# Kernel optimization log

Measured on AMD Instinct MI355X. Metric: run time of the kernel, lower is better.

Reference implementation:

```python
import jax, jax.numpy as jnp
import numpy as np
from jax import lax

VOCAB, H, B, T = 2514, 300, 128, 512

def setup_inputs() -> dict:
    key = jax.random.key(0)
    ks = jax.random.split(key, 12)
    s = 1.0 / np.sqrt(H)
    inp = {
        'x': jax.random.randint(ks[0], (B, T), 0, VOCAB),
        'emb': jax.random.normal(ks[1], (VOCAB, H), jnp.float32),
        'Wih0': jax.random.uniform(ks[2], (4 * H, H), jnp.float32, -s, s),
        'Whh0': jax.random.uniform(ks[3], (4 * H, H), jnp.float32, -s, s),
        'bih0': jax.random.uniform(ks[4], (4 * H,), jnp.float32, -s, s),
        'bhh0': jax.random.uniform(ks[5], (4 * H,), jnp.float32, -s, s),
        'Wih1': jax.random.uniform(ks[6], (4 * H, H), jnp.float32, -s, s),
        'Whh1': jax.random.uniform(ks[7], (4 * H, H), jnp.float32, -s, s),
        'bih1': jax.random.uniform(ks[8], (4 * H,), jnp.float32, -s, s),
        'bhh1': jax.random.uniform(ks[9], (4 * H,), jnp.float32, -s, s),
        'Wout': jax.random.uniform(ks[10], (VOCAB, H), jnp.float32, -s, s),
        'bout': jax.random.uniform(ks[11], (VOCAB,), jnp.float32, -s, s),
    }
    return inp


def lstm_layer(x, Wih, Whh, bih, bhh):
    # x: [B, T, H] -> [B, T, H]. PyTorch gate order: i, f, g, o.
    b, t, _ = x.shape
    h = Whh.shape[1]
    xg = jnp.einsum('bti,gi->btg', x, Wih) + (bih + bhh)  # [B, T, 4H]
    h0 = jnp.zeros((b, h), x.dtype)
    c0 = jnp.zeros((b, h), x.dtype)

    def step(carry, g_t):
        hp, cp = carry
        gates = g_t + hp @ Whh.T
        i, f, g, o = jnp.split(gates, 4, axis=-1)
        c = jax.nn.sigmoid(f) * cp + jax.nn.sigmoid(i) * jnp.tanh(g)
        hh = jax.nn.sigmoid(o) * jnp.tanh(c)
        return (hh, c), hh

    _, ys = lax.scan(step, (h0, c0), jnp.swapaxes(xg, 0, 1))  # [T, B, H]
    return jnp.swapaxes(ys, 0, 1)


def reference(x, emb, Wih0, Whh0, bih0, bhh0, Wih1, Whh1, bih1, bhh1, Wout, bout):
    e = emb[x]                                   # [B, T, H]
    h1 = lstm_layer(e, Wih0, Whh0, bih0, bhh0)   # layer 1
    h2 = lstm_layer(h1, Wih1, Whh1, bih1, bhh1)  # layer 2
    logits = jnp.einsum('bth,vh->btv', h2, Wout) + bout
    return logits.reshape(-1, logits.shape[-1])  # [B*T, VOCAB]
```

## Files before the change

kernel.cpp:

```cpp
#include <hip/hip_runtime.h>
#include <cstdint>
#include <cstddef>

namespace {

constexpr int H    = 300;
constexpr int B    = 128;
constexpr int T    = 512;
constexpr int NVOC = 2514;
constexpr int KP   = 304;

typedef __attribute__((ext_vector_type(8))) short  short8;
typedef __attribute__((ext_vector_type(4))) float  f32x4;

__device__ __forceinline__ float sigm(float x)     { return 1.f / (1.f + __expf(-x)); }
__device__ __forceinline__ float tanhfast(float x) { return 1.f - 2.f / (__expf(2.f*x) + 1.f); }

__device__ __forceinline__ unsigned short bf16_rn(float f) {
    unsigned u = __float_as_uint(f);
    u += 0x7FFFu + ((u >> 16) & 1u);
    return (unsigned short)(u >> 16);
}
__device__ __forceinline__ float bf16_f(unsigned short s) {
    return __uint_as_float(((unsigned)s) << 16);
}
__device__ __forceinline__ unsigned pack_hl(float v) {
    const unsigned short hi = bf16_rn(v);
    const unsigned short lo = bf16_rn(v - bf16_f(hi));
    return (unsigned)hi | ((unsigned)lo << 16);
}

constexpr int TSEG = 15 * 128 * 20;

constexpr unsigned SENTP = 0x7FB07FB0u;

__global__ __launch_bounds__(256)
void sentinel_fill(uint4* __restrict__ p, size_t n4)
{
    const uint4 s = make_uint4(SENTP, SENTP, SENTP, SENTP);
    size_t i = (size_t)blockIdx.x * blockDim.x + threadIdx.x;
    const size_t stride = (size_t)gridDim.x * blockDim.x;
    for (; i < n4; i += stride) p[i] = s;
}

__global__ __launch_bounds__(256)
void preconv(const float* __restrict__ src, unsigned* __restrict__ dst, int rows)
{
    const size_t n = (size_t)rows * KP;
    for (size_t i = (size_t)blockIdx.x * 256 + threadIdx.x; i < n;
         i += (size_t)gridDim.x * 256) {
        const int c = (int)(i % KP), r = (int)(i / KP);
        dst[i] = (c < H) ? pack_hl(src[(size_t)r * H + c]) : 0u;
    }
}

__global__ __launch_bounds__(256)
void gemm_pk(const unsigned* __restrict__ Apk, const unsigned* __restrict__ Wpk,
             const float* __restrict__ b1, float* __restrict__ out, int N)
{
    __shared__ __align__(16) unsigned short Ah[128][40], Al[128][40];
    __shared__ __align__(16) unsigned short Wh[128][40];

    const int tid = threadIdx.x;
    const int tt = blockIdx.y;
    const int n0 = blockIdx.x * 128;
    const int rl = tid >> 1, cb = (tid & 1) * 16;

    const unsigned* aptr = Apk + (size_t)tt * TSEG + rl * 20;
    const int nrow = n0 + rl;
    const unsigned* wptr = Wpk + (size_t)nrow * KP;
    const bool nok = (nrow < N);

    const int wv = tid >> 6, lane = tid & 63;
    const int mw = (wv >> 1) * 64, nw = (wv & 1) * 64;
    const int kg = lane >> 4, mm = lane & 15;

    f32x4 acc[4][4];
#pragma unroll
    for (int i = 0; i < 4; ++i)
#pragma unroll
        for (int j = 0; j < 4; ++j) acc[i][j] = (f32x4){0.f, 0.f, 0.f, 0.f};

    for (int kt = 0; kt < 10; ++kt) {
        uint4 pa[4], pw[4];
#pragma unroll
        for (int j = 0; j < 4; ++j) {
            const int col = kt * 32 + cb + j * 4;
            pa[j] = (col < 300)
                  ? *(const uint4*)(aptr + (col / 20) * 2560 + col % 20)
                  : make_uint4(0, 0, 0, 0);
            pw[j] = (nok && col < KP) ? *(const uint4*)(wptr + col)
                                      : make_uint4(0, 0, 0, 0);
        }
        __syncthreads();
#pragma unroll
        for (int j = 0; j < 4; ++j) {
            const int cc = cb + j * 4;
            *(uint2*)&Ah[rl][cc] = make_uint2((pa[j].x & 0xFFFFu) | (pa[j].y << 16),
                                              (pa[j].z & 0xFFFFu) | (pa[j].w << 16));
            *(uint2*)&Al[rl][cc] = make_uint2((pa[j].x >> 16) | (pa[j].y & 0xFFFF0000u),
                                              (pa[j].z >> 16) | (pa[j].w & 0xFFFF0000u));
            *(uint2*)&Wh[rl][cc] = make_uint2((pw[j].x & 0xFFFFu) | (pw[j].y << 16),
                                              (pw[j].z & 0xFFFFu) | (pw[j].w << 16));
        }
        __syncthreads();

        short8 fah[4], fal[4], fbh[4];
#pragma unroll
        for (int f = 0; f < 4; ++f) {
            fah[f] = *(const short8*)&Ah[mw + f*16 + mm][kg*8];
            fal[f] = *(const short8*)&Al[mw + f*16 + mm][kg*8];
            fbh[f] = *(const short8*)&Wh[nw + f*16 + mm][kg*8];
        }
#pragma unroll
        for (int mf = 0; mf < 4; ++mf)
#pragma unroll
            for (int nf = 0; nf < 4; ++nf) {
                acc[mf][nf] = __builtin_amdgcn_mfma_f32_16x16x32_bf16(fah[mf], fbh[nf], acc[mf][nf], 0, 0, 0);
                acc[mf][nf] = __builtin_amdgcn_mfma_f32_16x16x32_bf16(fal[mf], fbh[nf], acc[mf][nf], 0, 0, 0);
            }
    }

    float bias[4];
#pragma unroll
    for (int nf = 0; nf < 4; ++nf) {
        const int n = n0 + nw + nf*16 + mm;
        bias[nf] = (n < N) ? b1[n] : 0.f;
    }
    const int qr = lane >> 4;
#pragma unroll
    for (int mf = 0; mf < 4; ++mf) {
        const int b0 = mw + mf*16 + qr*4;
        float* orow = out + ((size_t)b0 * T + tt) * N;
#pragma unroll
        for (int nf = 0; nf < 4; ++nf) {
            const int n = n0 + nw + nf*16 + mm;
            if (n < N) {
#pragma unroll
                for (int r = 0; r < 4; ++r)
                    orow[(size_t)r * T * N + n] = acc[mf][nf][r] + bias[nf];
            }
        }
    }
}

constexpr int HGC = 15;
constexpr int BGC = 16;
constexpr int NWG = HGC * BGC;
constexpr int A2OFF  = 20480;
constexpr int EOFF   = 40960;
constexpr int APARF  = 61440;
constexpr int GDOFF  = 2 * APARF;
constexpr int TOKOFF = GDOFF + 10*8*16*4;
constexpr int FLDS   = TOKOFF + 8*512*4;

struct StageCtx {
    size_t   src64[5];
    int      aoffHi[5];
    unsigned pend0;
};

__device__ __forceinline__ void stage_init(StageCtx& S, int lane, int bg,
                                           int base_hg, int nchunks, int region)
{
    const int words = nchunks * 80;
    S.pend0 = 0;
#pragma unroll
    for (int j = 0; j < 5; ++j) {
        const int s = lane + 64 * j;
        const bool ok = (s < words);
        const int chunk = ok ? s / 80 : 0, rem = ok ? s % 80 : 0;
        const int hg = base_hg + chunk;
        S.src64[j] = (size_t)(hg * 128 + bg * 8) * 10 + rem;
        const int u2 = rem * 2, b_loc = u2 / 20, u = u2 % 20;
        const int k = hg * 20 + u;
        S.aoffHi[j] = region + ((k >> 5) * 8 + ((k >> 3) & 3)) * 256
                    + b_loc * 16 + (k & 7) * 2;
        if (ok) S.pend0 |= 1u << j;
    }
}

__device__ __forceinline__ void stage_poll(const StageCtx& S,
                                           const unsigned* __restrict__ slice,
                                           unsigned char* Ap)
{
    const unsigned long long* s64 = (const unsigned long long*)slice;
    unsigned long long val[5];
    unsigned pend = S.pend0;
    while (__any(pend != 0)) {
        unsigned long long w[5];
#pragma unroll
        for (int j = 0; j < 5; ++j)
            if (pend & (1u << j))
                w[j] = __hip_atomic_load(s64 + S.src64[j], __ATOMIC_RELAXED,
                                         __HIP_MEMORY_SCOPE_AGENT);
#pragma unroll
        for (int j = 0; j < 5; ++j)
            if (pend & (1u << j)) {
                const unsigned long long x = w[j];
                if ((unsigned)x != SENTP && (unsigned)(x >> 32) != SENTP) {
                    val[j] = x; pend &= ~(1u << j);
                }
            }
    }
#pragma unroll
    for (int j = 0; j < 5; ++j)
        if (S.pend0 & (1u << j)) {
            const unsigned p0 = (unsigned)val[j], p1 = (unsigned)(val[j] >> 32);
            *(unsigned*)(Ap + S.aoffHi[j])        = (p0 & 0xFFFFu) | (p1 << 16);
            *(unsigned*)(Ap + S.aoffHi[j] + 1024) = (p0 >> 16) | (p1 & 0xFFFF0000u);
        }
}

struct ECtx { int b[3]; int koff[3]; int aoff[3]; bool ok[3]; };

__device__ __forceinline__ void estage_init(ECtx& E, int tid)
{
#pragma unroll
    for (int j = 0; j < 3; ++j) {
        const int es = tid + 512 * j;
        E.ok[j] = (es < 1216);
        const int bb = E.ok[j] ? es / 152 : 0;
        const int kp = E.ok[j] ? es % 152 : 0;
        const int k  = kp * 2;
        E.b[j]    = bb;
        E.koff[j] = k;
        E.aoff[j] = EOFF + ((k >> 5) * 8 + ((k >> 3) & 3)) * 256
                  + bb * 16 + (k & 7) * 2;
    }
}

__device__ __forceinline__ void estage(const ECtx& E, const int* __restrict__ tokL,
                                       const unsigned* __restrict__ embcv, int it,
                                       unsigned char* Ap)
{
#pragma unroll
    for (int j = 0; j < 3; ++j)
        if (E.ok[j]) {
            const int tok = tokL[E.b[j] * 512 + it];
            const unsigned long long w = *(const unsigned long long*)
                (embcv + (size_t)tok * KP + E.koff[j]);
            const unsigned p0 = (unsigned)w, p1 = (unsigned)(w >> 32);
            *(unsigned*)(Ap + E.aoff[j])        = (p0 & 0xFFFFu) | (p1 << 16);
            *(unsigned*)(Ap + E.aoff[j] + 1024) = (p0 >> 16) | (p1 & 0xFFFF0000u);
        }
}

__device__ void fused_L0(int lane, int nt, int hg, int bg,
                         const unsigned* __restrict__ embcv,
                         const float* __restrict__ Wih0,
                         const float* __restrict__ Whh0,
                         const float* __restrict__ bih0,
                         const float* __restrict__ bhh0,
                         unsigned* __restrict__ h1p,
                         const unsigned* __restrict__ ssrc, int sreg, int sbase,
                         int snch, int sdel,
                         const ECtx& E, const int* __restrict__ tokL,
                         unsigned char* __restrict__ Abuf, float (*gd)[8][16])
{
    const int kg = lane >> 4, mm = lane & 15;

    short8 bhh[10], bih[10], bil[10];
#pragma unroll
    for (int kt = 0; kt < 10; ++kt) {
        const int c = nt * 16 + mm;
        const int grow = (c & 3) * H + hg * 20 + (c >> 2);
        short8 h_, ih_, il_;
#pragma unroll
        for (int e = 0; e < 8; ++e) {
            const int k = kt * 32 + kg * 8 + e;
            const float vh = (k < H) ? Whh0[(size_t)grow * H + k] : 0.f;
            const float vi = (k < H) ? Wih0[(size_t)grow * H + k] : 0.f;
            h_[e] = (short)bf16_rn(vh);
            const unsigned short i16 = bf16_rn(vi);
            ih_[e] = (short)i16;
            il_[e] = (short)bf16_rn(vi - bf16_f(i16));
        }
        bhh[kt] = h_; bih[kt] = ih_; bil[kt] = il_;
    }

    StageCtx S; stage_init(S, lane, bg, sbase, snch, sreg);

    const bool upd = lane < 32;
    const int b_u = lane >> 2, u4 = lane & 3;
    const int u_loc = nt * 4 + u4;
    float bias[4];
#pragma unroll
    for (int g = 0; g < 4; ++g)
        bias[g] = bih0[g * H + hg * 20 + u_loc] + bhh0[g * H + hg * 20 + u_loc];
    float cst = 0.f;
    unsigned* hst = h1p + ((size_t)hg * 128 + bg * 8 + b_u) * 20 + u_loc;

    for (int it = 0; it <= T; ++it) {
        unsigned char* Ap = Abuf + (it & 1) * APARF;
        if (it < T) estage(E, tokL, embcv, it, Ap);
        if (it >= sdel) stage_poll(S, ssrc + (size_t)(it - sdel) * TSEG, Ap);
        __syncthreads();

        if (it < T) {
            f32x4 acc = (f32x4){0.f, 0.f, 0.f, 0.f};
#pragma unroll
            for (int kt = 0; kt < 10; ++kt) {
                const int boff = (kt * 8 + kg) * 256 + mm * 16;
                const short8 eh = *(const short8*)(Ap + EOFF + boff);
                const short8 el = *(const short8*)(Ap + EOFF + boff + 1024);
                const short8 hh = *(const short8*)(Ap + boff);
                const short8 hl = *(const short8*)(Ap + boff + 1024);
                acc = __builtin_amdgcn_mfma_f32_16x16x32_bf16(eh, bih[kt], acc, 0, 0, 0);
                acc = __builtin_amdgcn_mfma_f32_16x16x32_bf16(el, bih[kt], acc, 0, 0, 0);
                acc = __builtin_amdgcn_mfma_f32_16x16x32_bf16(eh, bil[kt], acc, 0, 0, 0);
                acc = __builtin_amdgcn_mfma_f32_16x16x32_bf16(hh, bhh[kt], acc, 0, 0, 0);
                acc = __builtin_amdgcn_mfma_f32_16x16x32_bf16(hl, bhh[kt], acc, 0, 0, 0);
            }
            if (lane < 32) {
                const int br = (lane >> 4) * 4;
#pragma unroll
                for (int r = 0; r < 4; ++r) gd[nt][br + r][mm] = acc[r];
            }
            if (upd) {
                const float* g4 = &gd[nt][b_u][u4 * 4];
                const float gi = bias[0] + g4[0], gf = bias[1] + g4[1];
                const float gz = bias[2] + g4[2], go = bias[3] + g4[3];
                const float iG = sigm(gi), fG = sigm(gf);
                const float zG = tanhfast(gz), oG = sigm(go);
                cst = fmaf(fG, cst, iG * zG);
                const float hv = oG * tanhfast(cst);
                __hip_atomic_store(hst + (size_t)it * TSEG, pack_hl(hv),
                                   __ATOMIC_RELAXED, __HIP_MEMORY_SCOPE_AGENT);
            }
        }
    }
}

template<int NTL>
__device__ void fused_L1(int lane, int t0, int hg, int bg,
                         const unsigned* __restrict__ embcv,
                         const float* __restrict__ Wih1,
                         const float* __restrict__ Whh1,
                         const float* __restrict__ bih1,
                         const float* __restrict__ bhh1,
                         unsigned* __restrict__ h2p,
                         const unsigned* __restrict__ ssrc, int sreg, int sbase,
                         int snch, int sdel,
                         const ECtx& E, const int* __restrict__ tokL,
                         unsigned char* __restrict__ Abuf, float (*gd)[8][16])
{
    const int kg = lane >> 4, mm = lane & 15;

    short8 bi[NTL][10], bh[NTL][10];
#pragma unroll
    for (int t = 0; t < NTL; ++t)
#pragma unroll
        for (int kt = 0; kt < 10; ++kt) {
            const int c = (t0 + t) * 16 + mm;
            const int grow = (c & 3) * H + hg * 20 + (c >> 2);
            short8 i_, h_;
#pragma unroll
            for (int e = 0; e < 8; ++e) {
                const int k = kt * 32 + kg * 8 + e;
                i_[e] = (short)bf16_rn((k < H) ? Wih1[(size_t)grow * H + k] : 0.f);
                h_[e] = (short)bf16_rn((k < H) ? Whh1[(size_t)grow * H + k] : 0.f);
            }
            bi[t][kt] = i_; bh[t][kt] = h_;
        }

    StageCtx S; stage_init(S, lane, bg, sbase, snch, sreg);

    const bool upd = lane < NTL * 32;
    const int tile = lane >> 5, lidx = lane & 31;
    const int b_u = lidx >> 2, u4 = lidx & 3;
    const int ntg = t0 + ((NTL > 1) ? tile : 0);
    const int u_loc = ntg * 4 + u4;
    float bias[4];
#pragma unroll
    for (int g = 0; g < 4; ++g)
        bias[g] = bih1[g * H + hg * 20 + u_loc] + bhh1[g * H + hg * 20 + u_loc];
    float cst = 0.f;
    unsigned* hst = h2p + ((size_t)hg * 128 + bg * 8 + b_u) * 20 + u_loc;

    for (int it = 0; it <= T; ++it) {
        unsigned char* Ap = Abuf + (it & 1) * APARF;
        if (it < T) estage(E, tokL, embcv, it, Ap);
        if (it >= sdel) stage_poll(S, ssrc + (size_t)(it - sdel) * TSEG, Ap);
        __syncthreads();

        if (it >= 1) {
            f32x4 acc[NTL];
#pragma unroll
            for (int t = 0; t < NTL; ++t) acc[t] = (f32x4){0.f, 0.f, 0.f, 0.f};
#pragma unroll
            for (int kt = 0; kt < 10; ++kt) {
                const int boff = (kt * 8 + kg) * 256 + mm * 16;
                const short8 x1h = *(const short8*)(Ap + boff);
                const short8 x1l = *(const short8*)(Ap + boff + 1024);
                const short8 x2h = *(const short8*)(Ap + A2OFF + boff);
                const short8 x2l = *(const short8*)(Ap + A2OFF + boff + 1024);
#pragma unroll
                for (int t = 0; t < NTL; ++t) {
                    acc[t] = __builtin_amdgcn_mfma_f32_16x16x32_bf16(x1h, bi[t][kt], acc[t], 0, 0, 0);
                    acc[t] = __builtin_amdgcn_mfma_f32_16x16x32_bf16(x1l, bi[t][kt], acc[t], 0, 0, 0);
                    acc[t] = __builtin_amdgcn_mfma_f32_16x16x32_bf16(x2h, bh[t][kt], acc[t], 0, 0, 0);
                    acc[t] = __builtin_amdgcn_mfma_f32_16x16x32_bf16(x2l, bh[t][kt], acc[t], 0, 0, 0);
                }
            }
            if (lane < 32) {
                const int br = (lane >> 4) * 4;
#pragma unroll
                for (int t = 0; t < NTL; ++t)
#pragma unroll
                    for (int r = 0; r < 4; ++r) gd[5 + t0 + t][br + r][mm] = acc[t][r];
            }
            if (upd) {
                const float* g4 = &gd[5 + ntg][b_u][u4 * 4];
                const float gi = bias[0] + g4[0], gf = bias[1] + g4[1];
                const float gz = bias[2] + g4[2], go = bias[3] + g4[3];
                const float iG = sigm(gi), fG = sigm(gf);
                const float zG = tanhfast(gz), oG = sigm(go);
                cst = fmaf(fG, cst, iG * zG);
                const float hv = oG * tanhfast(cst);
                __hip_atomic_store(hst + (size_t)(it - 1) * TSEG, pack_hl(hv),
                                   __ATOMIC_RELAXED, __HIP_MEMORY_SCOPE_AGENT);
            }
        }
    }
}

__global__ __launch_bounds__(512, 2)
void lstm_fused(const int* __restrict__ x,
                const unsigned* __restrict__ embcv,
                const float* __restrict__ Wih0, const float* __restrict__ Whh0,
                const float* __restrict__ bih0, const float* __restrict__ bhh0,
                const float* __restrict__ Wih1, const float* __restrict__ Whh1,
                const float* __restrict__ bih1, const float* __restrict__ bhh1,
                unsigned* __restrict__ h1p, unsigned* __restrict__ h2p)
{
    extern __shared__ unsigned char smem[];
    unsigned char* Abuf = smem;
    float (*gd)[8][16] = (float(*)[8][16])(smem + GDOFF);
    int* tokL = (int*)(smem + TOKOFF);

    const int tid = threadIdx.x, wv = tid >> 6, lane = tid & 63;
    const int hg = blockIdx.x % HGC, bg = blockIdx.x / HGC;

    for (int i = tid; i < FLDS / 16; i += 512)
        ((uint4*)smem)[i] = make_uint4(0, 0, 0, 0);
    __syncthreads();
    for (int idx = tid; idx < 8 * 512; idx += 512) {
        const int b = idx >> 9, tt = idx & 511;
        tokL[idx] = x[(size_t)(bg * 8 + b) * T + tt];
    }
    __syncthreads();

    ECtx E; estage_init(E, tid);

    const int      sreg  = (wv < 4) ? 0 : A2OFF;
    const unsigned* ssrc = (wv < 4) ? h1p : h2p;
    const int      sbase = (wv & 3) * 4;
    const int      snch  = ((wv & 3) == 3) ? 3 : 4;
    const int      sdel  = (wv < 4) ? 1 : 2;

    if (wv < 5)
        fused_L0(lane, wv, hg, bg, embcv, Wih0, Whh0, bih0, bhh0, h1p,
                 ssrc, sreg, sbase, snch, sdel, E, tokL, Abuf, gd);
    else if (wv == 5)
        fused_L1<2>(lane, 0, hg, bg, embcv, Wih1, Whh1, bih1, bhh1, h2p,
                    ssrc, sreg, sbase, snch, sdel, E, tokL, Abuf, gd);
    else if (wv == 6)
        fused_L1<2>(lane, 2, hg, bg, embcv, Wih1, Whh1, bih1, bhh1, h2p,
                    ssrc, sreg, sbase, snch, sdel, E, tokL, Abuf, gd);
    else
        fused_L1<1>(lane, 4, hg, bg, embcv, Wih1, Whh1, bih1, bhh1, h2p,
                    ssrc, sreg, sbase, snch, sdel, E, tokL, Abuf, gd);
}

}

extern "C" void kernel_launch(void* const* d_in, const int* in_sizes, int n_in,
                              void* d_out, int out_size, void* d_ws, size_t ws_size,
                              hipStream_t stream)
{
    const int*   x    = (const int*)  d_in[0];
    const float* emb  = (const float*)d_in[1];
    const float* Wih0 = (const float*)d_in[2];
    const float* Whh0 = (const float*)d_in[3];
    const float* bih0 = (const float*)d_in[4];
    const float* bhh0 = (const float*)d_in[5];
    const float* Wih1 = (const float*)d_in[6];
    const float* Whh1 = (const float*)d_in[7];
    const float* bih1 = (const float*)d_in[8];
    const float* bhh1 = (const float*)d_in[9];
    const float* Wout = (const float*)d_in[10];
    const float* bout = (const float*)d_in[11];

    float* out = (float*)d_out;

    unsigned* h1p   = (unsigned*)d_ws;
    unsigned* h2p   = h1p + (size_t)T * TSEG;
    unsigned* embcv = h2p + (size_t)T * TSEG;
    unsigned* wcvo  = embcv + (size_t)NVOC * KP;

    const size_t nh4 = 2 * (size_t)T * TSEG / 4;
    sentinel_fill<<<dim3(2048), dim3(256), 0, stream>>>((uint4*)h1p, nh4);
    preconv<<<dim3(256), dim3(256), 0, stream>>>(emb,  embcv, NVOC);
    preconv<<<dim3(256), dim3(256), 0, stream>>>(Wout, wcvo,  NVOC);

    hipFuncSetAttribute(reinterpret_cast<const void*>(lstm_fused),
                        hipFuncAttributeMaxDynamicSharedMemorySize, FLDS);

    lstm_fused<<<dim3(NWG), dim3(512), FLDS, stream>>>(
        x, embcv, Wih0, Whh0, bih0, bhh0, Wih1, Whh1, bih1, bhh1, h1p, h2p);

    gemm_pk<<<dim3(20, 512), dim3(256), 0, stream>>>(h2p, wcvo, bout, out, NVOC);
}
```

Baseline: 3.061 ms.

## Fuse output projection GEMM into persistent LSTM kernel as per-step tail

Removes the separate output-projection GEMM launch. Each workgroup of the persistent LSTM kernel now computes the logits for its batch group and a slice of the vocabulary right after each timestep, reading the layer-2 hidden state already staged in shared memory. The Wout operand is stored as hi-only bf16 padded to 320 columns for direct MFMA fragment loads. This aims to overlap the projection with the serial recurrence and skip reloading h2 from global memory. The cost is extra per-step work and global output writes inside the latency-critical recurrent loop, plus two extra loop iterations.

```diff
diff --git a/kernel.cpp b/kernel.cpp
--- a/kernel.cpp
+++ b/kernel.cpp
@@ -9,6 +9,8 @@
 constexpr int T    = 512;
 constexpr int NVOC = 2514;
 constexpr int KP   = 304;
+constexpr int NTT  = 158;
+constexpr int NVP  = NTT * 16;
 
 typedef __attribute__((ext_vector_type(8))) short  short8;
 typedef __attribute__((ext_vector_type(4))) float  f32x4;
@@ -55,92 +57,14 @@
 }
 
 __global__ __launch_bounds__(256)
-void gemm_pk(const unsigned* __restrict__ Apk, const unsigned* __restrict__ Wpk,
-             const float* __restrict__ b1, float* __restrict__ out, int N)
-{
-    __shared__ __align__(16) unsigned short Ah[128][40], Al[128][40];
-    __shared__ __align__(16) unsigned short Wh[128][40];
-
-    const int tid = threadIdx.x;
-    const int tt = blockIdx.y;
-    const int n0 = blockIdx.x * 128;
-    const int rl = tid >> 1, cb = (tid & 1) * 16;
-
-    const unsigned* aptr = Apk + (size_t)tt * TSEG + rl * 20;
-    const int nrow = n0 + rl;
-    const unsigned* wptr = Wpk + (size_t)nrow * KP;
-    const bool nok = (nrow < N);
-
-    const int wv = tid >> 6, lane = tid & 63;
-    const int mw = (wv >> 1) * 64, nw = (wv & 1) * 64;
-    const int kg = lane >> 4, mm = lane & 15;
-
-    f32x4 acc[4][4];
-#pragma unroll
-    for (int i = 0; i < 4; ++i)
-#pragma unroll
-        for (int j = 0; j < 4; ++j) acc[i][j] = (f32x4){0.f, 0.f, 0.f, 0.f};
-
-    for (int kt = 0; kt < 10; ++kt) {
-        uint4 pa[4], pw[4];
-#pragma unroll
-        for (int j = 0; j < 4; ++j) {
-            const int col = kt * 32 + cb + j * 4;
-            pa[j] = (col < 300)
-                  ? *(const uint4*)(aptr + (col / 20) * 2560 + col % 20)
-                  : make_uint4(0, 0, 0, 0);
-            pw[j] = (nok && col < KP) ? *(const uint4*)(wptr + col)
-                                      : make_uint4(0, 0, 0, 0);
-        }
-        __syncthreads();
-#pragma unroll
-        for (int j = 0; j < 4; ++j) {
-            const int cc = cb + j * 4;
-            *(uint2*)&Ah[rl][cc] = make_uint2((pa[j].x & 0xFFFFu) | (pa[j].y << 16),
-                                              (pa[j].z & 0xFFFFu) | (pa[j].w << 16));
-            *(uint2*)&Al[rl][cc] = make_uint2((pa[j].x >> 16) | (pa[j].y & 0xFFFF0000u),
-                                              (pa[j].z >> 16) | (pa[j].w & 0xFFFF0000u));
-            *(uint2*)&Wh[rl][cc] = make_uint2((pw[j].x & 0xFFFFu) | (pw[j].y << 16),
-                                              (pw[j].z & 0xFFFFu) | (pw[j].w << 16));
-        }
-        __syncthreads();
-
-        short8 fah[4], fal[4], fbh[4];
-#pragma unroll
-        for (int f = 0; f < 4; ++f) {
-            fah[f] = *(const short8*)&Ah[mw + f*16 + mm][kg*8];
-            fal[f] = *(const short8*)&Al[mw + f*16 + mm][kg*8];
-            fbh[f] = *(const short8*)&Wh[nw + f*16 + mm][kg*8];
-        }
-#pragma unroll
-        for (int mf = 0; mf < 4; ++mf)
-#pragma unroll
-            for (int nf = 0; nf < 4; ++nf) {
-                acc[mf][nf] = __builtin_amdgcn_mfma_f32_16x16x32_bf16(fah[mf], fbh[nf], acc[mf][nf], 0, 0, 0);
-                acc[mf][nf] = __builtin_amdgcn_mfma_f32_16x16x32_bf16(fal[mf], fbh[nf], acc[mf][nf], 0, 0, 0);
-            }
-    }
-
-    float bias[4];
-#pragma unroll
-    for (int nf = 0; nf < 4; ++nf) {
-        const int n = n0 + nw + nf*16 + mm;
-        bias[nf] = (n < N) ? b1[n] : 0.f;
-    }
-    const int qr = lane >> 4;
-#pragma unroll
-    for (int mf = 0; mf < 4; ++mf) {
-        const int b0 = mw + mf*16 + qr*4;
-        float* orow = out + ((size_t)b0 * T + tt) * N;
-#pragma unroll
-        for (int nf = 0; nf < 4; ++nf) {
-            const int n = n0 + nw + nf*16 + mm;
-            if (n < N) {
-#pragma unroll
-                for (int r = 0; r < 4; ++r)
-                    orow[(size_t)r * T * N + n] = acc[mf][nf][r] + bias[nf];
-            }
-        }
+void preconv_hi(const float* __restrict__ src, unsigned short* __restrict__ dst,
+                int rows)
+{
+    const size_t n = (size_t)NVP * 320;
+    for (size_t i = (size_t)blockIdx.x * 256 + threadIdx.x; i < n;
+         i += (size_t)gridDim.x * 256) {
+        const int c = (int)(i % 320), r = (int)(i / 320);
+        dst[i] = (r < rows && c < H) ? bf16_rn(src[(size_t)r * H + c]) : 0;
     }
 }
 
@@ -246,7 +170,47 @@
         }
 }
 
-__device__ void fused_L0(int lane, int nt, int hg, int bg,
+__device__ __forceinline__ void gemm_tail(int lane, int wvid, int hg, int bg,
+                                          int it,
+                                          const unsigned short* __restrict__ wcvh,
+                                          const float* __restrict__ bout,
+                                          float* __restrict__ out,
+                                          const unsigned char* __restrict__ Abuf)
+{
+    const int s = it - 2;
+    const unsigned char* Ap = Abuf + (it & 1) * APARF + A2OFF;
+    const int kg = lane >> 4, mm = lane & 15;
+    const int nt0 = (hg * NTT) / HGC, nt1 = ((hg + 1) * NTT) / HGC;
+
+#pragma unroll
+    for (int rep = 0; rep < 2; ++rep) {
+        const int nt = nt0 + wvid + rep * 8;
+        if (nt < nt1) {
+            const int n = nt * 16 + mm;
+            const unsigned short* wrow = wcvh + (size_t)n * 320 + kg * 8;
+            f32x4 acc = (f32x4){0.f, 0.f, 0.f, 0.f};
+#pragma unroll
+            for (int kt = 0; kt < 10; ++kt) {
+                const short8 wf = *(const short8*)(wrow + kt * 32);
+                const int boff = (kt * 8 + kg) * 256 + mm * 16;
+                const short8 ah = *(const short8*)(Ap + boff);
+                const short8 al = *(const short8*)(Ap + boff + 1024);
+                acc = __builtin_amdgcn_mfma_f32_16x16x32_bf16(ah, wf, acc, 0, 0, 0);
+                acc = __builtin_amdgcn_mfma_f32_16x16x32_bf16(al, wf, acc, 0, 0, 0);
+            }
+            const int row = (lane >> 4) * 4;
+            if (row < 8 && n < NVOC) {
+                const float bb = bout[n];
+#pragma unroll
+                for (int r = 0; r < 4; ++r)
+                    out[((size_t)(bg * 8 + row + r) * T + s) * NVOC + n] =
+                        acc[r] + bb;
+            }
+        }
+    }
+}
+
+__device__ void fused_L0(int lane, int wvid, int nt, int hg, int bg,
                          const unsigned* __restrict__ embcv,
                          const float* __restrict__ Wih0,
                          const float* __restrict__ Whh0,
@@ -256,6 +220,8 @@
                          const unsigned* __restrict__ ssrc, int sreg, int sbase,
                          int snch, int sdel,
                          const ECtx& E, const int* __restrict__ tokL,
+                         const unsigned short* __restrict__ wcvh,
+                         const float* __restrict__ bout, float* __restrict__ out,
                          unsigned char* __restrict__ Abuf, float (*gd)[8][16])
 {
     const int kg = lane >> 4, mm = lane & 15;
@@ -291,10 +257,11 @@
     float cst = 0.f;
     unsigned* hst = h1p + ((size_t)hg * 128 + bg * 8 + b_u) * 20 + u_loc;
 
-    for (int it = 0; it <= T; ++it) {
+    for (int it = 0; it <= T + 1; ++it) {
         unsigned char* Ap = Abuf + (it & 1) * APARF;
         if (it < T) estage(E, tokL, embcv, it, Ap);
-        if (it >= sdel) stage_poll(S, ssrc + (size_t)(it - sdel) * TSEG, Ap);
+        if (it >= sdel && it - sdel < T)
+            stage_poll(S, ssrc + (size_t)(it - sdel) * TSEG, Ap);
         __syncthreads();
 
         if (it < T) {
@@ -329,11 +296,12 @@
                                    __ATOMIC_RELAXED, __HIP_MEMORY_SCOPE_AGENT);
             }
         }
+        if (it >= 2) gemm_tail(lane, wvid, hg, bg, it, wcvh, bout, out, Abuf);
     }
 }
 
 template<int NTL>
-__device__ void fused_L1(int lane, int t0, int hg, int bg,
+__device__ void fused_L1(int lane, int wvid, int t0, int hg, int bg,
                          const unsigned* __restrict__ embcv,
                          const float* __restrict__ Wih1,
                          const float* __restrict__ Whh1,
@@ -343,6 +311,8 @@
                          const unsigned* __restrict__ ssrc, int sreg, int sbase,
                          int snch, int sdel,
                          const ECtx& E, const int* __restrict__ tokL,
+                         const unsigned short* __restrict__ wcvh,
+                         const float* __restrict__ bout, float* __restrict__ out,
                          unsigned char* __restrict__ Abuf, float (*gd)[8][16])
 {
     const int kg = lane >> 4, mm = lane & 15;
@@ -378,13 +348,14 @@
     float cst = 0.f;
     unsigned* hst = h2p + ((size_t)hg * 128 + bg * 8 + b_u) * 20 + u_loc;
 
-    for (int it = 0; it <= T; ++it) {
+    for (int it = 0; it <= T + 1; ++it) {
         unsigned char* Ap = Abuf + (it & 1) * APARF;
         if (it < T) estage(E, tokL, embcv, it, Ap);
-        if (it >= sdel) stage_poll(S, ssrc + (size_t)(it - sdel) * TSEG, Ap);
+        if (it >= sdel && it - sdel < T)
+            stage_poll(S, ssrc + (size_t)(it - sdel) * TSEG, Ap);
         __syncthreads();
 
-        if (it >= 1) {
+        if (it >= 1 && it <= T) {
             f32x4 acc[NTL];
 #pragma unroll
             for (int t = 0; t < NTL; ++t) acc[t] = (f32x4){0.f, 0.f, 0.f, 0.f};
@@ -422,6 +393,7 @@
                                    __ATOMIC_RELAXED, __HIP_MEMORY_SCOPE_AGENT);
             }
         }
+        if (it >= 2) gemm_tail(lane, wvid, hg, bg, it, wcvh, bout, out, Abuf);
     }
 }
 
@@ -432,7 +404,9 @@
                 const float* __restrict__ bih0, const float* __restrict__ bhh0,
                 const float* __restrict__ Wih1, const float* __restrict__ Whh1,
                 const float* __restrict__ bih1, const float* __restrict__ bhh1,
-                unsigned* __restrict__ h1p, unsigned* __restrict__ h2p)
+                unsigned* __restrict__ h1p, unsigned* __restrict__ h2p,
+                const unsigned short* __restrict__ wcvh,
+                const float* __restrict__ bout, float* __restrict__ out)
 {
     extern __shared__ unsigned char smem[];
     unsigned char* Abuf = smem;
@@ -460,17 +434,21 @@
     const int      sdel  = (wv < 4) ? 1 : 2;
 
     if (wv < 5)
-        fused_L0(lane, wv, hg, bg, embcv, Wih0, Whh0, bih0, bhh0, h1p,
-                 ssrc, sreg, sbase, snch, sdel, E, tokL, Abuf, gd);
+        fused_L0(lane, wv, wv, hg, bg, embcv, Wih0, Whh0, bih0, bhh0, h1p,
+                 ssrc, sreg, sbase, snch, sdel, E, tokL, wcvh, bout, out,
+                 Abuf, gd);
     else if (wv == 5)
-        fused_L1<2>(lane, 0, hg, bg, embcv, Wih1, Whh1, bih1, bhh1, h2p,
-                    ssrc, sreg, sbase, snch, sdel, E, tokL, Abuf, gd);
+        fused_L1<2>(lane, wv, 0, hg, bg, embcv, Wih1, Whh1, bih1, bhh1, h2p,
+                    ssrc, sreg, sbase, snch, sdel, E, tokL, wcvh, bout, out,
+                    Abuf, gd);
     else if (wv == 6)
-        fused_L1<2>(lane, 2, hg, bg, embcv, Wih1, Whh1, bih1, bhh1, h2p,
-                    ssrc, sreg, sbase, snch, sdel, E, tokL, Abuf, gd);
+        fused_L1<2>(lane, wv, 2, hg, bg, embcv, Wih1, Whh1, bih1, bhh1, h2p,
+                    ssrc, sreg, sbase, snch, sdel, E, tokL, wcvh, bout, out,
+                    Abuf, gd);
     else
-        fused_L1<1>(lane, 4, hg, bg, embcv, Wih1, Whh1, bih1, bhh1, h2p,
-                    ssrc, sreg, sbase, snch, sdel, E, tokL, Abuf, gd);
+        fused_L1<1>(lane, wv, 4, hg, bg, embcv, Wih1, Whh1, bih1, bhh1, h2p,
+                    ssrc, sreg, sbase, snch, sdel, E, tokL, wcvh, bout, out,
+                    Abuf, gd);
 }
 
 }
@@ -497,18 +475,17 @@
     unsigned* h1p   = (unsigned*)d_ws;
     unsigned* h2p   = h1p + (size_t)T * TSEG;
     unsigned* embcv = h2p + (size_t)T * TSEG;
-    unsigned* wcvo  = embcv + (size_t)NVOC * KP;
+    unsigned short* wcvh = (unsigned short*)(embcv + (size_t)NVOC * KP);
 
     const size_t nh4 = 2 * (size_t)T * TSEG / 4;
     sentinel_fill<<<dim3(2048), dim3(256), 0, stream>>>((uint4*)h1p, nh4);
-    preconv<<<dim3(256), dim3(256), 0, stream>>>(emb,  embcv, NVOC);
-    preconv<<<dim3(256), dim3(256), 0, stream>>>(Wout, wcvo,  NVOC);
+    preconv<<<dim3(256), dim3(256), 0, stream>>>(emb, embcv, NVOC);
+    preconv_hi<<<dim3(256), dim3(256), 0, stream>>>(Wout, wcvh, NVOC);
 
     hipFuncSetAttribute(reinterpret_cast<const void*>(lstm_fused),
                         hipFuncAttributeMaxDynamicSharedMemorySize, FLDS);
 
     lstm_fused<<<dim3(NWG), dim3(512), FLDS, stream>>>(
-        x, embcv, Wih0, Whh0, bih0, bhh0, Wih1, Whh1, bih1, bhh1, h1p, h2p);
-
-    gemm_pk<<<dim3(20, 512), dim3(256), 0, stream>>>(h2p, wcvo, bout, out, NVOC);
-}
+        x, embcv, Wih0, Whh0, bih0, bhh0, Wih1, Whh1, bih1, bhh1,
+        h1p, h2p, wcvh, bout, out);
+}
```

After: 5.346 ms. 1.75x slower.
